# Kernel optimization log

Measured on AMD Instinct MI355X. Metric: run time of the kernel, lower is better.

The kernel has to match this reference:

```python
import jax, jax.numpy as jnp
import numpy as np

B, N, D = 4, 1024, 1024
H, HD, G = 16, 64, 4          # num_heads, dim_heads, num_groups
KVH = H // G                   # kv heads = 4


def setup_inputs() -> dict:
    key = jax.random.key(0)
    ks = jax.random.split(key, 5)
    s = 0.02
    return {
        "x": jax.random.normal(ks[0], (B, N, D), jnp.float32),
        "Wq": jax.random.normal(ks[1], (D, H * HD), jnp.float32) * s,
        "Wkv": jax.random.normal(ks[2], (D, 2 * H * HD // G), jnp.float32) * s,
        "Wg": jax.random.normal(ks[3], (D, H * HD), jnp.float32) * s,
        "bg": jnp.zeros((H * HD,), jnp.float32),
        "Wo": jax.random.normal(ks[4], (H * HD, D), jnp.float32) * s,
    }


def reference(x, Wq, Wkv, Wg, bg, Wo):
    # QKV projections (no bias on q/kv/o; bias on gate)
    q = (x @ Wq).reshape(B, N, H, HD).transpose(0, 2, 1, 3)        # (B,H,N,HD)
    kv = x @ Wkv                                                    # (B,N,2*KVH*HD)
    k, v = jnp.split(kv, 2, axis=-1)
    k = k.reshape(B, N, KVH, HD).transpose(0, 2, 1, 3)             # (B,KVH,N,HD)
    v = v.reshape(B, N, KVH, HD).transpose(0, 2, 1, 3)
    # GQA: repeat_interleave kv heads to match query heads
    k = jnp.repeat(k, G, axis=1)                                    # (B,H,N,HD)
    v = jnp.repeat(v, G, axis=1)
    # scaled dot product attention
    scores = jnp.einsum("bhqd,bhkd->bhqk", q, k) / jnp.sqrt(jnp.float32(HD))
    attn = jax.nn.softmax(scores, axis=-1)
    out = jnp.einsum("bhqk,bhkd->bhqd", attn, v)                    # (B,H,N,HD)
    out = out.transpose(0, 2, 1, 3).reshape(B, N, H * HD)
    # elementwise gate then output projection
    gate = x @ Wg + bg
    return (gate * out) @ Wo
```

## Files before the change

### kernel.cpp

```cpp
#include <hip/hip_runtime.h>
#include <hip/hip_bf16.h>
#include <stdint.h>

#define BB 4
#define NN 1024
#define DD 1024
#define HH 16
#define HDIM 64
#define KVHH 4
#define MM (BB * NN)

typedef __hip_bfloat16 bf16;
typedef __attribute__((ext_vector_type(8))) short bf16x8;
typedef __attribute__((ext_vector_type(4))) float f32x4;

__device__ __forceinline__ float b2f(unsigned short u) {
  return __uint_as_float(((unsigned)u) << 16);
}
__device__ __forceinline__ unsigned short f2b(float x) {
  bf16 h = __float2bfloat16(x);
  unsigned short u;
  __builtin_memcpy(&u, &h, 2);
  return u;
}
__device__ __forceinline__ f32x4 mfma16(bf16x8 a, bf16x8 b, f32x4 c) {
  return __builtin_amdgcn_mfma_f32_16x16x32_bf16(a, b, c, 0, 0, 0);
}
__device__ __forceinline__ void gl_lds16(const short* g, short* l) {
  __builtin_amdgcn_global_load_lds(
      (const __attribute__((address_space(1))) unsigned*)g,
      (__attribute__((address_space(3))) unsigned*)l, 16, 0, 0);
}

__global__ __launch_bounds__(256) void transpose_all(
    const float* __restrict__ Wq, const float* __restrict__ Wkv,
    const float* __restrict__ Wg, const float* __restrict__ Wo,
    const float* __restrict__ bg, const float* __restrict__ x,
    short* __restrict__ WcT, short* __restrict__ WoT,
    float* __restrict__ bias, short* __restrict__ xb) {
  const int z = blockIdx.z;
  if (z == 4) {
    if (blockIdx.y == 0 && blockIdx.x < 10) {
      int i = blockIdx.x * 256 + threadIdx.x;
      if (i < 2560) bias[i] = (i >= 1024 && i < 2048) ? bg[i - 1024] : 0.f;
    }
    return;
  }
  if (z == 5) {
    int base = (blockIdx.y * 16 + blockIdx.x) * 256 + threadIdx.x;
#pragma unroll
    for (int it = 0; it < 16; ++it) {
      int i = base + it * 65536;
      float4 v = *(const float4*)&x[(size_t)i * 4];
      ushort4 o;
      o.x = f2b(v.x); o.y = f2b(v.y); o.z = f2b(v.z); o.w = f2b(v.w);
      *(ushort4*)&xb[(size_t)i * 4] = o;
    }
    return;
  }
  const float* W;
  short* WT;
  int N = 1024;
  const int K = 1024;
  if (z == 0) { W = Wq; WT = WcT; }
  else if (z == 1) { W = Wg; WT = WcT + 1048576; }
  else if (z == 2) {
    W = Wkv; WT = WcT + 2097152; N = 512;
    if (blockIdx.x >= 8) return;
  } else { W = Wo; WT = WoT; }

  __shared__ short T[64 * 68];
  const int tid = threadIdx.x;
  const int n0 = blockIdx.x * 64, k0 = blockIdx.y * 64;
  {
    int i0 = tid >> 4, j4 = (tid & 15) * 4;
#pragma unroll
    for (int ii = 0; ii < 4; ++ii) {
      int i = i0 + 16 * ii;
      float4 w = *(const float4*)&W[(size_t)(k0 + i) * N + n0 + j4];
      ushort4 o;
      o.x = f2b(w.x); o.y = f2b(w.y); o.z = f2b(w.z); o.w = f2b(w.w);
      *(ushort4*)&T[i * 68 + j4] = o;
    }
  }
  __syncthreads();
  {
    int n = tid >> 2, k16 = (tid & 3) * 16;
    short tmp[16];
#pragma unroll
    for (int kk = 0; kk < 16; ++kk) tmp[kk] = T[(k16 + kk) * 68 + n];
    short* dst = WT + (size_t)(n0 + n) * K + k0 + k16;
#pragma unroll
    for (int s = 0; s < 16; s += 4) *(ushort4*)&dst[s] = *(const ushort4*)&tmp[s];
  }
}

__global__ __launch_bounds__(256, 5) void gemm_proj(
    const short* __restrict__ A, const short* __restrict__ WT,
    const float* __restrict__ bias, short* __restrict__ qc,
    short* __restrict__ gc, short* __restrict__ kc, short* __restrict__ vt) {
  __shared__ short As[2][64 * 32];
  __shared__ short Bs[2][128 * 32];
  const int tid = threadIdx.x;
  const int wave = tid >> 6, lane = tid & 63, l15 = lane & 15, quad = lane >> 4;
  const int m0 = blockIdx.y * 64, n0 = blockIdx.x * 128;
  const int wm = (wave & 1) * 32, wn = (wave >> 1) * 64;
  const int arow = tid >> 2, ac = (tid & 3) * 8;
  const short* asrc = A + (size_t)(m0 + arow) * 1024 + ac;
  const short* bsrc = WT + (size_t)(n0 + arow) * 1024 + ac;

  gl_lds16(asrc, &As[0][wave * 512]);
  gl_lds16(bsrc, &Bs[0][wave * 512]);
  gl_lds16(bsrc + 64 * 1024, &Bs[0][wave * 512 + 2048]);

  f32x4 acc[2][4] = {};
  for (int k = 0; k < 32; ++k) {
    const int cur = k & 1;
    __syncthreads();
    if (k < 31) {
      const short* ap = asrc + (k + 1) * 32;
      const short* bp = bsrc + (k + 1) * 32;
      gl_lds16(ap, &As[1 - cur][wave * 512]);
      gl_lds16(bp, &Bs[1 - cur][wave * 512]);
      gl_lds16(bp + 64 * 1024, &Bs[1 - cur][wave * 512 + 2048]);
    }
    bf16x8 af[2], bfr[4];
#pragma unroll
    for (int i = 0; i < 2; ++i)
      af[i] = *(const bf16x8*)&As[cur][(wm + 16 * i + l15) * 32 + quad * 8];
#pragma unroll
    for (int j = 0; j < 4; ++j)
      bfr[j] = *(const bf16x8*)&Bs[cur][(wn + 16 * j + l15) * 32 + quad * 8];
#pragma unroll
    for (int i = 0; i < 2; ++i)
#pragma unroll
      for (int j = 0; j < 4; ++j) acc[i][j] = mfma16(af[i], bfr[j], acc[i][j]);
  }
#pragma unroll
  for (int j = 0; j < 4; ++j) {
    int col = n0 + wn + 16 * j + l15;
    float bv = bias[col];
    int reg = col >> 6;
    int d = col & 63;
#pragma unroll
    for (int i = 0; i < 2; ++i) {
#pragma unroll
      for (int r = 0; r < 4; ++r) {
        int row = m0 + wm + 16 * i + quad * 4 + r;
        int b = row >> 10, tok = row & 1023;
        unsigned short v = f2b(acc[i][j][r] + bv);
        if (reg < 16)
          ((unsigned short*)qc)[((size_t)((b * 16 + reg) * 1024 + tok)) * 64 + d] = v;
        else if (reg < 32)
          ((unsigned short*)gc)[((size_t)((b * 16 + reg - 16) * 1024 + tok)) * 64 + d] = v;
        else if (reg < 36)
          ((unsigned short*)kc)[((size_t)((b * 4 + reg - 32) * 1024 + tok)) * 64 + d] = v;
        else
          ((unsigned short*)vt)[((size_t)((b * 4 + reg - 36) * 64 + d)) * 1024 + tok] = v;
      }
    }
  }
}

__global__ __launch_bounds__(256, 4) void gemm_out(
    const short* __restrict__ A, const short* __restrict__ WT,
    float* __restrict__ Cout) {
  __shared__ short As[2][64 * 32];
  __shared__ short Bs[2][64 * 32];
  const int tid = threadIdx.x;
  const int wave = tid >> 6, lane = tid & 63, l15 = lane & 15, quad = lane >> 4;
  const int m0 = blockIdx.y * 64, n0 = blockIdx.x * 64;
  const int wm = (wave & 1) * 32, wn = (wave >> 1) * 32;
  const int arow = tid >> 2, ac = (tid & 3) * 8;
  const short* asrc = A + (size_t)(m0 + arow) * 1024 + ac;
  const short* bsrc = WT + (size_t)(n0 + arow) * 1024 + ac;

  gl_lds16(asrc, &As[0][wave * 512]);
  gl_lds16(bsrc, &Bs[0][wave * 512]);

  f32x4 acc[2][2] = {};
  for (int k = 0; k < 32; ++k) {
    const int cur = k & 1;
    __syncthreads();
    if (k < 31) {
      gl_lds16(asrc + (k + 1) * 32, &As[1 - cur][wave * 512]);
      gl_lds16(bsrc + (k + 1) * 32, &Bs[1 - cur][wave * 512]);
    }
    bf16x8 af[2], bfr[2];
#pragma unroll
    for (int i = 0; i < 2; ++i)
      af[i] = *(const bf16x8*)&As[cur][(wm + 16 * i + l15) * 32 + quad * 8];
#pragma unroll
    for (int j = 0; j < 2; ++j)
      bfr[j] = *(const bf16x8*)&Bs[cur][(wn + 16 * j + l15) * 32 + quad * 8];
#pragma unroll
    for (int i = 0; i < 2; ++i)
#pragma unroll
      for (int j = 0; j < 2; ++j) acc[i][j] = mfma16(af[i], bfr[j], acc[i][j]);
  }
#pragma unroll
  for (int j = 0; j < 2; ++j) {
    int col = n0 + wn + 16 * j + l15;
#pragma unroll
    for (int i = 0; i < 2; ++i) {
#pragma unroll
      for (int r = 0; r < 4; ++r) {
        int row = m0 + wm + 16 * i + quad * 4 + r;
        Cout[(size_t)row * 1024 + col] = acc[i][j][r];
      }
    }
  }
}

__global__ __launch_bounds__(256, 4) void attn_mfma8(
    const short* __restrict__ qc, const short* __restrict__ gc,
    const short* __restrict__ kc, const short* __restrict__ vt,
    unsigned short* __restrict__ gated) {
  __shared__ short Ps[2][64 * 64];
  __shared__ float Lpart[4 * 64];
  __shared__ float Lq[64];
  const int tid = threadIdx.x;
  const int w = tid >> 6, lane = tid & 63, l15 = lane & 15, quad = lane >> 4;
  const int qt = blockIdx.x, bh = blockIdx.y, b = bh >> 4, h = bh & 15, kvh = h >> 2;
  const int fs = l15 & 7;
  const int s0 = (quad ^ fs) * 8;
  const int s1 = ((4 + quad) ^ fs) * 8;
  const int pslot = ((2 * w + (quad >> 1)) ^ fs) * 8 + (quad & 1) * 4;

  bf16x8 qf[4][2];
#pragma unroll
  for (int jq = 0; jq < 4; ++jq) {
    const short* qp =
        qc + ((size_t)((b * 16 + h) * 1024) + qt * 64 + 16 * jq + l15) * 64 + quad * 8;
    qf[jq][0] = *(const bf16x8*)qp;
    qf[jq][1] = *(const bf16x8*)(qp + 32);
  }

  const short* kb = kc + ((size_t)((b * 4 + kvh) * 1024) + 16 * w + l15) * 64 + quad * 8;
  const short* vb = vt + ((size_t)((b * 4 + kvh) * 64) + 16 * w + l15) * 1024 + quad * 8;

  f32x4 oacc[4];
  float ls[4];
#pragma unroll
  for (int jq = 0; jq < 4; ++jq) {
    oacc[jq] = (f32x4){0.f, 0.f, 0.f, 0.f};
    ls[jq] = 0.f;
  }

  bf16x8 kfr[2][2], vfr[2][2];
  kfr[0][0] = *(const bf16x8*)(kb);
  kfr[0][1] = *(const bf16x8*)(kb + 32);
  vfr[0][0] = *(const bf16x8*)(vb);
  vfr[0][1] = *(const bf16x8*)(vb + 32);

  for (int kt = 0; kt < 16; ++kt) {
    const int pb = kt & 1, nb = pb ^ 1;
    if (kt < 15) {
      const short* kp = kb + (size_t)(kt + 1) * 4096;
      const short* vp = vb + (size_t)(kt + 1) * 64;
      kfr[nb][0] = *(const bf16x8*)(kp);
      kfr[nb][1] = *(const bf16x8*)(kp + 32);
      vfr[nb][0] = *(const bf16x8*)(vp);
      vfr[nb][1] = *(const bf16x8*)(vp + 32);
    }
    short* ps = &Ps[pb][0];
#pragma unroll
    for (int jq = 0; jq < 4; ++jq) {
      f32x4 st = mfma16(kfr[pb][0], qf[jq][0], (f32x4){0.f, 0.f, 0.f, 0.f});
      st = mfma16(kfr[pb][1], qf[jq][1], st);
      float p0 = exp2f(st[0] * 0.18033688f);
      float p1 = exp2f(st[1] * 0.18033688f);
      float p2 = exp2f(st[2] * 0.18033688f);
      float p3 = exp2f(st[3] * 0.18033688f);
      ls[jq] += (p0 + p1) + (p2 + p3);
      uint2 dd;
      dd.x = (unsigned)f2b(p0) | ((unsigned)f2b(p1) << 16);
      dd.y = (unsigned)f2b(p2) | ((unsigned)f2b(p3) << 16);
      *(uint2*)&ps[(16 * jq + l15) * 64 + pslot] = dd;
    }
    __syncthreads();
#pragma unroll
    for (int jq = 0; jq < 4; ++jq) {
      bf16x8 pf0 = *(const bf16x8*)&ps[(16 * jq + l15) * 64 + s0];
      bf16x8 pf1 = *(const bf16x8*)&ps[(16 * jq + l15) * 64 + s1];
      oacc[jq] = mfma16(pf0, vfr[pb][0], oacc[jq]);
      oacc[jq] = mfma16(pf1, vfr[pb][1], oacc[jq]);
    }
  }

#pragma unroll
  for (int jq = 0; jq < 4; ++jq) {
    ls[jq] += __shfl_xor(ls[jq], 16);
    ls[jq] += __shfl_xor(ls[jq], 32);
  }
  if (quad == 0) {
#pragma unroll
    for (int jq = 0; jq < 4; ++jq) Lpart[w * 64 + 16 * jq + l15] = ls[jq];
  }
  __syncthreads();
  if (tid < 64)
    Lq[tid] = Lpart[tid] + Lpart[64 + tid] + Lpart[128 + tid] + Lpart[192 + tid];
  __syncthreads();

#pragma unroll
  for (int jq = 0; jq < 4; ++jq) {
#pragma unroll
    for (int r = 0; r < 4; ++r) {
      int qloc = 16 * jq + 4 * quad + r;
      float lv = Lq[qloc];
      float gv = b2f(((const unsigned short*)gc)[
          ((size_t)((b * 16 + h) * 1024) + qt * 64 + qloc) * 64 + 16 * w + l15]);
      size_t row = (size_t)(b * NN + qt * 64 + qloc);
      gated[row * 1024 + h * 64 + 16 * w + l15] = f2b(oacc[jq][r] / lv * gv);
    }
  }
}

extern "C" void kernel_launch(void* const* d_in, const int* in_sizes, int n_in,
                              void* d_out, int out_size, void* d_ws,
                              size_t ws_size, hipStream_t stream) {
  const float* x = (const float*)d_in[0];
  const float* Wq = (const float*)d_in[1];
  const float* Wkv = (const float*)d_in[2];
  const float* Wg = (const float*)d_in[3];
  const float* bg = (const float*)d_in[4];
  const float* Wo = (const float*)d_in[5];
  float* out = (float*)d_out;

  short* ws = (short*)d_ws;
  short* xb = ws;
  short* WcT = xb + 4194304;
  short* WoT = WcT + 2621440;
  short* qc = WoT + 1048576;
  short* gc = qc + 4194304;
  short* kc = gc + 4194304;
  short* vtw = kc + 1048576;
  float* bias_f32 = (float*)(vtw + 1048576);

  dim3 blk(256);
  transpose_all<<<dim3(16, 16, 6), blk, 0, stream>>>(Wq, Wkv, Wg, Wo, bg, x,
                                                     WcT, WoT, bias_f32, xb);
  gemm_proj<<<dim3(20, 64), blk, 0, stream>>>(xb, WcT, bias_f32, qc, gc, kc, vtw);
  attn_mfma8<<<dim3(16, 64), blk, 0, stream>>>(qc, gc, kc, vtw, (unsigned short*)xb);
  gemm_out<<<dim3(16, 64), blk, 0, stream>>>(xb, WoT, out);
}
```

Measured before the change: 188.0 us.

## Keep softmax probabilities in registers and feed PV MFMA directly, reducing partial outputs at end

The attention kernel no longer writes P to shared memory and syncs every key tile. The S tile's accumulator layout is reused as the B operand of a 16x16x16 bf16 MFMA against V, so each wave holds partial O for all 64 dims over its own key slice. The four wave partials are summed through two padded fp32 LDS buffers at the end. This removes the per-iteration barrier and the LDS round trip for P, at the cost of 4x more output accumulator registers, lower occupancy (launch bound 3) and smaller K=16 MFMAs.

```diff
diff --git a/kernel.cpp b/kernel.cpp
--- a/kernel.cpp
+++ b/kernel.cpp
@@ -12,6 +12,7 @@
 
 typedef __hip_bfloat16 bf16;
 typedef __attribute__((ext_vector_type(8))) short bf16x8;
+typedef __attribute__((ext_vector_type(4))) short bf16x4;
 typedef __attribute__((ext_vector_type(4))) float f32x4;
 
 __device__ __forceinline__ float b2f(unsigned short u) {
@@ -25,6 +26,16 @@
 }
 __device__ __forceinline__ f32x4 mfma16(bf16x8 a, bf16x8 b, f32x4 c) {
   return __builtin_amdgcn_mfma_f32_16x16x32_bf16(a, b, c, 0, 0, 0);
+}
+__device__ __forceinline__ f32x4 mfma16k16(bf16x4 a, bf16x4 b, f32x4 c) {
+#if __has_builtin(__builtin_amdgcn_mfma_f32_16x16x16bf16_1k)
+  return __builtin_amdgcn_mfma_f32_16x16x16bf16_1k(a, b, c, 0, 0, 0);
+#else
+  asm volatile("s_nop 1\n\tv_mfma_f32_16x16x16_bf16 %0, %1, %2, %0"
+               : "+v"(c)
+               : "v"(a), "v"(b));
+  return c;
+#endif
 }
 __device__ __forceinline__ void gl_lds16(const short* g, short* l) {
   __builtin_amdgcn_global_load_lds(
@@ -212,20 +223,17 @@
   }
 }
 
-__global__ __launch_bounds__(256, 4) void attn_mfma8(
+__global__ __launch_bounds__(256, 3) void attn_mfma9(
     const short* __restrict__ qc, const short* __restrict__ gc,
     const short* __restrict__ kc, const short* __restrict__ vt,
     unsigned short* __restrict__ gated) {
-  __shared__ short Ps[2][64 * 64];
+  __shared__ float OA[64 * 65];
+  __shared__ float OB[64 * 65];
   __shared__ float Lpart[4 * 64];
   __shared__ float Lq[64];
   const int tid = threadIdx.x;
   const int w = tid >> 6, lane = tid & 63, l15 = lane & 15, quad = lane >> 4;
   const int qt = blockIdx.x, bh = blockIdx.y, b = bh >> 4, h = bh & 15, kvh = h >> 2;
-  const int fs = l15 & 7;
-  const int s0 = (quad ^ fs) * 8;
-  const int s1 = ((4 + quad) ^ fs) * 8;
-  const int pslot = ((2 * w + (quad >> 1)) ^ fs) * 8 + (quad & 1) * 4;
 
   bf16x8 qf[4][2];
 #pragma unroll
@@ -237,33 +245,29 @@
   }
 
   const short* kb = kc + ((size_t)((b * 4 + kvh) * 1024) + 16 * w + l15) * 64 + quad * 8;
-  const short* vb = vt + ((size_t)((b * 4 + kvh) * 64) + 16 * w + l15) * 1024 + quad * 8;
-
-  f32x4 oacc[4];
-  float ls[4];
-#pragma unroll
-  for (int jq = 0; jq < 4; ++jq) {
-    oacc[jq] = (f32x4){0.f, 0.f, 0.f, 0.f};
-    ls[jq] = 0.f;
-  }
-
-  bf16x8 kfr[2][2], vfr[2][2];
+  const short* vb = vt + ((size_t)((b * 4 + kvh) * 64 + l15)) * 1024 + 16 * w + quad * 4;
+
+  f32x4 oacc[4][4] = {};
+  float ls[4] = {0.f, 0.f, 0.f, 0.f};
+
+  bf16x8 kfr[2][2];
+  bf16x4 vfr[2][4];
   kfr[0][0] = *(const bf16x8*)(kb);
   kfr[0][1] = *(const bf16x8*)(kb + 32);
-  vfr[0][0] = *(const bf16x8*)(vb);
-  vfr[0][1] = *(const bf16x8*)(vb + 32);
+#pragma unroll
+  for (int dt = 0; dt < 4; ++dt) vfr[0][dt] = *(const bf16x4*)(vb + dt * 16384);
 
   for (int kt = 0; kt < 16; ++kt) {
     const int pb = kt & 1, nb = pb ^ 1;
     if (kt < 15) {
       const short* kp = kb + (size_t)(kt + 1) * 4096;
-      const short* vp = vb + (size_t)(kt + 1) * 64;
+      const short* vp = vb + (kt + 1) * 64;
       kfr[nb][0] = *(const bf16x8*)(kp);
       kfr[nb][1] = *(const bf16x8*)(kp + 32);
-      vfr[nb][0] = *(const bf16x8*)(vp);
-      vfr[nb][1] = *(const bf16x8*)(vp + 32);
-    }
-    short* ps = &Ps[pb][0];
+#pragma unroll
+      for (int dt = 0; dt < 4; ++dt)
+        vfr[nb][dt] = *(const bf16x4*)(vp + dt * 16384);
+    }
 #pragma unroll
     for (int jq = 0; jq < 4; ++jq) {
       f32x4 st = mfma16(kfr[pb][0], qf[jq][0], (f32x4){0.f, 0.f, 0.f, 0.f});
@@ -273,18 +277,14 @@
       float p2 = exp2f(st[2] * 0.18033688f);
       float p3 = exp2f(st[3] * 0.18033688f);
       ls[jq] += (p0 + p1) + (p2 + p3);
-      uint2 dd;
-      dd.x = (unsigned)f2b(p0) | ((unsigned)f2b(p1) << 16);
-      dd.y = (unsigned)f2b(p2) | ((unsigned)f2b(p3) << 16);
-      *(uint2*)&ps[(16 * jq + l15) * 64 + pslot] = dd;
-    }
-    __syncthreads();
-#pragma unroll
-    for (int jq = 0; jq < 4; ++jq) {
-      bf16x8 pf0 = *(const bf16x8*)&ps[(16 * jq + l15) * 64 + s0];
-      bf16x8 pf1 = *(const bf16x8*)&ps[(16 * jq + l15) * 64 + s1];
-      oacc[jq] = mfma16(pf0, vfr[pb][0], oacc[jq]);
-      oacc[jq] = mfma16(pf1, vfr[pb][1], oacc[jq]);
+      bf16x4 pbf;
+      pbf[0] = (short)f2b(p0);
+      pbf[1] = (short)f2b(p1);
+      pbf[2] = (short)f2b(p2);
+      pbf[3] = (short)f2b(p3);
+#pragma unroll
+      for (int dt = 0; dt < 4; ++dt)
+        oacc[jq][dt] = mfma16k16(vfr[pb][dt], pbf, oacc[jq][dt]);
     }
   }
 
@@ -297,21 +297,43 @@
 #pragma unroll
     for (int jq = 0; jq < 4; ++jq) Lpart[w * 64 + 16 * jq + l15] = ls[jq];
   }
+
+  float* Ob = (w & 1) ? OB : OA;
+  if (w < 2) {
+#pragma unroll
+    for (int jq = 0; jq < 4; ++jq)
+#pragma unroll
+      for (int dt = 0; dt < 4; ++dt)
+#pragma unroll
+        for (int r = 0; r < 4; ++r)
+          Ob[(16 * dt + 4 * quad + r) * 65 + 16 * jq + l15] = oacc[jq][dt][r];
+  }
   __syncthreads();
+  if (w >= 2) {
+#pragma unroll
+    for (int jq = 0; jq < 4; ++jq)
+#pragma unroll
+      for (int dt = 0; dt < 4; ++dt)
+#pragma unroll
+        for (int r = 0; r < 4; ++r)
+          Ob[(16 * dt + 4 * quad + r) * 65 + 16 * jq + l15] += oacc[jq][dt][r];
+  }
   if (tid < 64)
     Lq[tid] = Lpart[tid] + Lpart[64 + tid] + Lpart[128 + tid] + Lpart[192 + tid];
   __syncthreads();
 
+  const int d = 16 * w + l15;
 #pragma unroll
   for (int jq = 0; jq < 4; ++jq) {
 #pragma unroll
     for (int r = 0; r < 4; ++r) {
       int qloc = 16 * jq + 4 * quad + r;
+      float ov = OA[d * 65 + qloc] + OB[d * 65 + qloc];
       float lv = Lq[qloc];
       float gv = b2f(((const unsigned short*)gc)[
-          ((size_t)((b * 16 + h) * 1024) + qt * 64 + qloc) * 64 + 16 * w + l15]);
+          ((size_t)((b * 16 + h) * 1024) + qt * 64 + qloc) * 64 + d]);
       size_t row = (size_t)(b * NN + qt * 64 + qloc);
-      gated[row * 1024 + h * 64 + 16 * w + l15] = f2b(oacc[jq][r] / lv * gv);
+      gated[row * 1024 + h * 64 + d] = f2b(ov / lv * gv);
     }
   }
 }
@@ -341,6 +363,6 @@
   transpose_all<<<dim3(16, 16, 6), blk, 0, stream>>>(Wq, Wkv, Wg, Wo, bg, x,
                                                      WcT, WoT, bias_f32, xb);
   gemm_proj<<<dim3(20, 64), blk, 0, stream>>>(xb, WcT, bias_f32, qc, gc, kc, vtw);
-  attn_mfma8<<<dim3(16, 64), blk, 0, stream>>>(qc, gc, kc, vtw, (unsigned short*)xb);
+  attn_mfma9<<<dim3(16, 64), blk, 0, stream>>>(qc, gc, kc, vtw, (unsigned short*)xb);
   gemm_out<<<dim3(16, 64), blk, 0, stream>>>(xb, WoT, out);
 }
```

New measurement: 240.8 us. +28.1%, slower.
